# Performance work log

Measured on AMD Instinct MI355X. Metric: run time of the kernel, lower is better.

The kernel has to match this reference:

```python
import jax, jax.numpy as jnp
import numpy as np

N_HEAD = 16


def setup_inputs() -> dict:
    key = jax.random.key(0)
    ks = jax.random.split(key, 3)
    B, T, C = 4, 2048, 1024
    x = jax.random.normal(ks[0], (B, T, C), dtype=jnp.float32)
    w_attn = jax.random.normal(ks[1], (3 * C, C), dtype=jnp.float32) * (1.0 / np.sqrt(C))
    b_attn = jnp.zeros((3 * C,), dtype=jnp.float32)
    w_proj = jax.random.normal(ks[2], (C, C), dtype=jnp.float32) * (1.0 / np.sqrt(C))
    b_proj = jnp.zeros((C,), dtype=jnp.float32)
    return {"x": x, "w_attn": w_attn, "b_attn": b_attn, "w_proj": w_proj, "b_proj": b_proj}


def reference(x, w_attn, b_attn, w_proj, b_proj):
    B, T, C = x.shape
    H = N_HEAD
    D = C // H
    qkv = x @ w_attn.T + b_attn                      # [B, T, 3C]
    q, k, v = jnp.split(qkv, 3, axis=-1)
    # [B, T, C] -> [B, H, T, D]
    q = q.reshape(B, T, H, D).transpose(0, 2, 1, 3)
    k = k.reshape(B, T, H, D).transpose(0, 2, 1, 3)
    v = v.reshape(B, T, H, D).transpose(0, 2, 1, 3)
    scale = 1.0 / np.sqrt(D).astype(np.float32)
    att = jnp.einsum('bhqd,bhkd->bhqk', q, k) * scale  # [B, H, T, T]
    causal = jnp.tril(jnp.ones((T, T), dtype=bool))
    att = jnp.where(causal[None, None], att, -jnp.inf)
    att = jax.nn.softmax(att, axis=-1)
    y = jnp.einsum('bhqk,bhkd->bhqd', att, v)          # [B, H, T, D]
    y = y.transpose(0, 2, 1, 3).reshape(B, T, C)
    return y @ w_proj.T + b_proj
```

## Files before the change

kernel.cpp:

```cpp
#include <hip/hip_runtime.h>
#include <hip/hip_bf16.h>
#include <stdint.h>

typedef __attribute__((ext_vector_type(8))) short bf16x8;
typedef __attribute__((ext_vector_type(4))) float f32x4;

#define MFMA16(a, b, c) __builtin_amdgcn_mfma_f32_16x16x32_bf16((a), (b), (c), 0, 0, 0)

__device__ __forceinline__ unsigned short f2bf(float f) {
  unsigned int u = __builtin_bit_cast(unsigned int, f);
  unsigned int r = (u + 0x7fffu + ((u >> 16) & 1u)) >> 16;
  return (unsigned short)r;
}

__device__ __forceinline__ void gload16(const unsigned short* g, unsigned short* lds_dst) {
  __builtin_amdgcn_global_load_lds(
      (const __attribute__((address_space(1))) unsigned int*)g,
      (__attribute__((address_space(3))) unsigned int*)lds_dst, 16, 0, 0);
}

__global__ void cvt_f32_bf16(const float* __restrict__ in, unsigned short* __restrict__ out, long n) {
  long i = ((long)blockIdx.x * blockDim.x + threadIdx.x) * 4;
  long stride = (long)gridDim.x * blockDim.x * 4;
  for (; i < n; i += stride) {
    float4 v = *(const float4*)(in + i);
    ushort4 o;
    o.x = f2bf(v.x); o.y = f2bf(v.y); o.z = f2bf(v.z); o.w = f2bf(v.w);
    *(ushort4*)(out + i) = o;
  }
}

template <int EPI, int NB>
__global__ __launch_bounds__(512, 2)
void gemm_bt(const unsigned short* __restrict__ A,
             const unsigned short* __restrict__ Bt,
             const float* __restrict__ bias,
             int M, int N, int K,
             unsigned short* __restrict__ q_out,
             unsigned short* __restrict__ k_out,
             unsigned short* __restrict__ vt_out,
             float* __restrict__ f_out) {
  constexpr int BNT = NB * 64;
  alignas(16) __shared__ unsigned short Alds[2][2][128 * 64];
  alignas(16) __shared__ unsigned short Blds[2][BNT * 64];
  const int t = threadIdx.x, w = t >> 6, l = t & 63;
  const int bm = blockIdx.x, bn = blockIdx.y;
  const int wm = w >> 2, wn = w & 3;
  const int lo = l & 15, hi = l >> 4, swk = lo & 7;

  f32x4 acc[8][NB];
  const f32x4 zero = {0.f, 0.f, 0.f, 0.f};
#pragma unroll
  for (int i = 0; i < 8; ++i)
#pragma unroll
    for (int j = 0; j < NB; ++j) acc[i][j] = zero;

  const int sr = t >> 3;
  const int gsrcE = ((t & 7) ^ (sr & 7)) * 8;
  const unsigned short* Asrc = A + (long)(bm * 256 + sr) * K + gsrcE;
  const unsigned short* Bsrc = Bt + (long)(bn * BNT + sr) * K + gsrcE;

#define STAGE_AH(sb, qh, koff) do {                                    \
    unsigned short* d_ = &Alds[sb][qh][w * 512];                       \
    const unsigned short* s_ = Asrc + (long)(qh) * 64 * K + (koff);    \
    gload16(s_, d_); gload16(s_ + 128L * K, d_ + 4096); } while (0)
#define STAGE_B(sb, koff) do {                                         \
    _Pragma("unroll")                                                  \
    for (int c_ = 0; c_ < NB; ++c_)                                    \
      gload16(Bsrc + (long)c_ * 64 * K + (koff),                       \
              &Blds[sb][c_ * 4096 + w * 512]); } while (0)

  STAGE_AH(0, 0, 0);
  STAGE_AH(0, 1, 0);
  STAGE_B(0, 0);
  asm volatile("s_waitcnt vmcnt(0)" ::: "memory");
  __builtin_amdgcn_sched_barrier(0);
  __builtin_amdgcn_s_barrier();

  const int lrA = (wm * 64 + lo) * 64;
  const int lrB = (wn * (NB * 16) + lo) * 64;
  const int gk0 = ((hi) ^ swk) * 8;
  const int gk1 = ((4 + hi) ^ swk) * 8;

  bf16x8 af[4][2], blo[2][2], bhi[2];

  for (int kt = 0; kt < 16; ++kt) {
    const int c = kt & 1, nb = c ^ 1;
    const bool st = (kt < 15);
    const int koff = (kt + 1) * 64;
    const unsigned short* A0 = Alds[c][0];
    const unsigned short* A1 = Alds[c][1];
    const unsigned short* Bs = Blds[c];

#pragma unroll
    for (int ii = 0; ii < 4; ++ii) {
      af[ii][0] = *(const bf16x8*)&A0[lrA + ii * 1024 + gk0];
      af[ii][1] = *(const bf16x8*)&A0[lrA + ii * 1024 + gk1];
    }
#pragma unroll
    for (int jj = 0; jj < NB - 1; ++jj) {
      blo[jj][0] = *(const bf16x8*)&Bs[lrB + jj * 1024 + gk0];
      blo[jj][1] = *(const bf16x8*)&Bs[lrB + jj * 1024 + gk1];
    }
    if (st) STAGE_AH(nb, 0, koff);
    __builtin_amdgcn_s_barrier();
    asm volatile("s_waitcnt lgkmcnt(0)" ::: "memory");
    __builtin_amdgcn_sched_barrier(0);
    __builtin_amdgcn_s_setprio(1);
#pragma unroll
    for (int ii = 0; ii < 4; ++ii)
#pragma unroll
      for (int jj = 0; jj < NB - 1; ++jj) {
        acc[ii][jj] = MFMA16(af[ii][0], blo[jj][0], acc[ii][jj]);
        acc[ii][jj] = MFMA16(af[ii][1], blo[jj][1], acc[ii][jj]);
      }
    __builtin_amdgcn_s_setprio(0);
    __builtin_amdgcn_s_barrier();

    bhi[0] = *(const bf16x8*)&Bs[lrB + (NB - 1) * 1024 + gk0];
    bhi[1] = *(const bf16x8*)&Bs[lrB + (NB - 1) * 1024 + gk1];
    if (st) STAGE_AH(nb, 1, koff);
    __builtin_amdgcn_s_barrier();
    asm volatile("s_waitcnt lgkmcnt(0)" ::: "memory");
    __builtin_amdgcn_sched_barrier(0);
    __builtin_amdgcn_s_setprio(1);
#pragma unroll
    for (int ii = 0; ii < 4; ++ii) {
      acc[ii][NB - 1] = MFMA16(af[ii][0], bhi[0], acc[ii][NB - 1]);
      acc[ii][NB - 1] = MFMA16(af[ii][1], bhi[1], acc[ii][NB - 1]);
    }
    __builtin_amdgcn_s_setprio(0);
    __builtin_amdgcn_s_barrier();

#pragma unroll
    for (int ii = 0; ii < 4; ++ii) {
      af[ii][0] = *(const bf16x8*)&A1[lrA + ii * 1024 + gk0];
      af[ii][1] = *(const bf16x8*)&A1[lrA + ii * 1024 + gk1];
    }
    if (st) STAGE_B(nb, koff);
    __builtin_amdgcn_s_barrier();
    asm volatile("s_waitcnt lgkmcnt(0)" ::: "memory");
    __builtin_amdgcn_sched_barrier(0);
    __builtin_amdgcn_s_setprio(1);
#pragma unroll
    for (int ii = 0; ii < 4; ++ii) {
      acc[4 + ii][NB - 1] = MFMA16(af[ii][0], bhi[0], acc[4 + ii][NB - 1]);
      acc[4 + ii][NB - 1] = MFMA16(af[ii][1], bhi[1], acc[4 + ii][NB - 1]);
    }
    __builtin_amdgcn_s_setprio(0);
    __builtin_amdgcn_s_barrier();

    __builtin_amdgcn_s_setprio(1);
#pragma unroll
    for (int ii = 0; ii < 4; ++ii)
#pragma unroll
      for (int jj = 0; jj < NB - 1; ++jj) {
        acc[4 + ii][jj] = MFMA16(af[ii][0], blo[jj][0], acc[4 + ii][jj]);
        acc[4 + ii][jj] = MFMA16(af[ii][1], blo[jj][1], acc[4 + ii][jj]);
      }
    __builtin_amdgcn_s_setprio(0);
    if (st) {
      asm volatile("s_waitcnt vmcnt(0)" ::: "memory");
      __builtin_amdgcn_sched_barrier(0);
    }
    __builtin_amdgcn_s_barrier();
  }
#undef STAGE_AH
#undef STAGE_B

#pragma unroll
  for (int i = 0; i < 8; ++i) {
#pragma unroll
    for (int j = 0; j < NB; ++j) {
#pragma unroll
      for (int r = 0; r < 4; ++r) {
        int row = bm * 256 + wm * 128 + i * 16 + hi * 4 + r;
        int col = bn * BNT + wn * (NB * 16) + j * 16 + lo;
        float v = acc[i][j][r] + bias[col];
        if (EPI == 0) {
          int b = row >> 11, tt = row & 2047;
          int seg = col >> 10, cc = col & 1023;
          int h = cc >> 6, d = cc & 63;
          long bh = (long)(b * 16 + h);
          if (seg == 0)      q_out[(bh * 2048 + tt) * 64 + d] = f2bf(v * 0.1803368801111f);
          else if (seg == 1) k_out[(bh * 2048 + tt) * 64 + d] = f2bf(v);
          else               vt_out[(bh * 64 + d) * 2048 + tt] = f2bf(v);
        } else {
          f_out[(long)row * N + col] = v;
        }
      }
    }
  }
}

__global__ __launch_bounds__(512, 4)
void attn_kernel(const unsigned short* __restrict__ Q,
                 const unsigned short* __restrict__ K,
                 const unsigned short* __restrict__ Vt,
                 unsigned short* __restrict__ Y) {
  alignas(16) __shared__ unsigned short Kbuf[2][64 * 64];
  alignas(16) __shared__ unsigned short Vbuf[2][64 * 64];
  alignas(16) __shared__ unsigned short pbuf[8][16 * 64];
  const int t = threadIdx.x, w = t >> 6, l = t & 63;
  const int lo = l & 15, hi = l >> 4;
  const int bh = blockIdx.x;
  const int p = blockIdx.y;
  const int b = bh >> 4, h = bh & 15;
  const int sA = p, sB = 15 - p;
  const int nA = 2 * p + 2;
  const int nTot = 34;
  const unsigned short* Qp = Q + (long)bh * 2048 * 64;
  const unsigned short* Kp = K + (long)bh * 2048 * 64;
  const unsigned short* Vp = Vt + (long)bh * 64 * 2048;
  unsigned short* pw = pbuf[w];

  const short one_bf = (short)0x3F80;
  const bf16x8 ones = {one_bf, one_bf, one_bf, one_bf, one_bf, one_bf, one_bf, one_bf};
  const f32x4 zero = {0.f, 0.f, 0.f, 0.f};

  const int qbA = sA * 128 + w * 16;
  const int qbB = sB * 128 + w * 16;

  bf16x8 qf0, qf1;
  f32x4 lsum;
  f32x4 oacc[4];

  qf0 = *(const bf16x8*)&Qp[(qbA + lo) * 64 + hi * 8];
  qf1 = *(const bf16x8*)&Qp[(qbA + lo) * 64 + 32 + hi * 8];
  lsum = zero;
#pragma unroll
  for (int dg = 0; dg < 4; ++dg) oacc[dg] = zero;

  const int srow = t >> 3;
  const int scw = ((t & 7) ^ (srow & 7)) * 8;
  const int sw = lo & 7;

#define STAGE(kvoff, bufidx)                                          \
  do {                                                                \
    unsigned short* KB_ = Kbuf[bufidx] + w * 512;                     \
    unsigned short* VB_ = Vbuf[bufidx] + w * 512;                     \
    gload16(Kp + (long)((kvoff) + srow) * 64 + scw, KB_);             \
    gload16(Vp + (long)srow * 2048 + (kvoff) + scw, VB_);             \
  } while (0)

  STAGE(0, 0);
  __syncthreads();

  for (int g = 0; g < nTot; ++g) {
    const bool inA = (g < nA);
    const int kvb = (inA ? g : g - nA) * 64;
    const int cur = g & 1;
    if (g + 1 < nTot) {
      const int jn = (g + 1 < nA) ? g + 1 : g + 1 - nA;
      STAGE(jn * 64, cur ^ 1);
    }
    const int qbase = inA ? qbA : qbB;
    if (kvb <= qbase + 15) {
      const unsigned short* KB = Kbuf[cur];
      const unsigned short* VB = Vbuf[cur];
      f32x4 s[4];
#pragma unroll
      for (int cg = 0; cg < 4; ++cg) s[cg] = zero;
      __builtin_amdgcn_s_setprio(1);
#pragma unroll
      for (int cg = 0; cg < 4; ++cg) {
        bf16x8 k0 = *(const bf16x8*)&KB[(cg * 16 + lo) * 64 + ((hi) ^ sw) * 8];
        bf16x8 k1 = *(const bf16x8*)&KB[(cg * 16 + lo) * 64 + ((4 + hi) ^ sw) * 8];
        s[cg] = MFMA16(k0, qf0, s[cg]);
        s[cg] = MFMA16(k1, qf1, s[cg]);
      }
      __builtin_amdgcn_s_setprio(0);
      if (kvb + 63 > qbase) {
        const int limit = qbase + lo - kvb;
#pragma unroll
        for (int cg = 0; cg < 4; ++cg)
#pragma unroll
          for (int r = 0; r < 4; ++r)
            if (cg * 16 + hi * 4 + r > limit) s[cg][r] = -__builtin_inff();
      }
#pragma unroll
      for (int cg = 0; cg < 4; ++cg) {
        float p0 = exp2f(s[cg][0]);
        float p1 = exp2f(s[cg][1]);
        float p2 = exp2f(s[cg][2]);
        float p3 = exp2f(s[cg][3]);
        unsigned int u0, u1;
        asm("v_cvt_pk_bf16_f32 %0, %1, %2" : "=v"(u0) : "v"(p0), "v"(p1));
        asm("v_cvt_pk_bf16_f32 %0, %1, %2" : "=v"(u1) : "v"(p2), "v"(p3));
        const int gg = (cg * 2 + (hi >> 1)) ^ sw;
        uint2 val; val.x = u0; val.y = u1;
        *(uint2*)&pw[lo * 64 + gg * 8 + (hi & 1) * 4] = val;
      }
      asm volatile("s_waitcnt lgkmcnt(0)" ::: "memory");
      bf16x8 pa0 = *(const bf16x8*)&pw[lo * 64 + ((hi) ^ sw) * 8];
      bf16x8 pa1 = *(const bf16x8*)&pw[lo * 64 + ((4 + hi) ^ sw) * 8];
      __builtin_amdgcn_s_setprio(1);
      lsum = MFMA16(pa0, ones, lsum);
      lsum = MFMA16(pa1, ones, lsum);
#pragma unroll
      for (int dg = 0; dg < 4; ++dg) {
        bf16x8 vv0 = *(const bf16x8*)&VB[(dg * 16 + lo) * 64 + ((hi) ^ sw) * 8];
        bf16x8 vv1 = *(const bf16x8*)&VB[(dg * 16 + lo) * 64 + ((4 + hi) ^ sw) * 8];
        oacc[dg] = MFMA16(pa0, vv0, oacc[dg]);
        oacc[dg] = MFMA16(pa1, vv1, oacc[dg]);
      }
      __builtin_amdgcn_s_setprio(0);
    }
    if (g == nA - 1) {
#pragma unroll
      for (int r = 0; r < 4; ++r) {
        float inv = 1.0f / lsum[r];
        int rowg = qbA + hi * 4 + r;
        long base = ((long)b * 2048 + rowg) * 1024 + h * 64;
#pragma unroll
        for (int dg = 0; dg < 4; ++dg)
          Y[base + dg * 16 + lo] = f2bf(oacc[dg][r] * inv);
      }
      qf0 = *(const bf16x8*)&Qp[(qbB + lo) * 64 + hi * 8];
      qf1 = *(const bf16x8*)&Qp[(qbB + lo) * 64 + 32 + hi * 8];
      lsum = zero;
#pragma unroll
      for (int dg = 0; dg < 4; ++dg) oacc[dg] = zero;
    }
    __syncthreads();
  }

#pragma unroll
  for (int r = 0; r < 4; ++r) {
    float inv = 1.0f / lsum[r];
    int rowg = qbB + hi * 4 + r;
    long base = ((long)b * 2048 + rowg) * 1024 + h * 64;
#pragma unroll
    for (int dg = 0; dg < 4; ++dg)
      Y[base + dg * 16 + lo] = f2bf(oacc[dg][r] * inv);
  }
#undef STAGE
}

extern "C" void kernel_launch(void* const* d_in, const int* in_sizes, int n_in,
                              void* d_out, int out_size, void* d_ws, size_t ws_size,
                              hipStream_t stream) {
  const float* x      = (const float*)d_in[0];
  const float* w_attn = (const float*)d_in[1];
  const float* b_attn = (const float*)d_in[2];
  const float* w_proj = (const float*)d_in[3];
  const float* b_proj = (const float*)d_in[4];
  float* out = (float*)d_out;

  const long NX = 8192L * 1024;
  const long NWA = 3072L * 1024;
  const long NWP = 1024L * 1024;
  const long NQ = 64L * 2048 * 64;

  char* ws = (char*)d_ws;
  unsigned short* xb  = (unsigned short*)ws; ws += NX * 2;
  unsigned short* wab = (unsigned short*)ws; ws += NWA * 2;
  unsigned short* wpb = (unsigned short*)ws; ws += NWP * 2;
  unsigned short* qb  = (unsigned short*)ws; ws += NQ * 2;
  unsigned short* kb  = (unsigned short*)ws; ws += NQ * 2;
  unsigned short* vtb = (unsigned short*)ws; ws += NQ * 2;
  unsigned short* yb  = (unsigned short*)ws; ws += NX * 2;

  cvt_f32_bf16<<<2048, 256, 0, stream>>>(x, xb, NX);
  cvt_f32_bf16<<<768, 256, 0, stream>>>(w_attn, wab, NWA);
  cvt_f32_bf16<<<256, 256, 0, stream>>>(w_proj, wpb, NWP);

  dim3 g1(32, 16);
  gemm_bt<0, 3><<<g1, 512, 0, stream>>>(xb, wab, b_attn, 8192, 3072, 1024,
                                        qb, kb, vtb, nullptr);
  dim3 ga(64, 8);
  attn_kernel<<<ga, 512, 0, stream>>>(qb, kb, vtb, yb);
  dim3 g2(32, 8);
  gemm_bt<1, 2><<<g2, 512, 0, stream>>>(yb, wpb, b_proj, 8192, 1024, 1024,
                                        nullptr, nullptr, nullptr, out);
}
```

Before: 181.7 us.

## Shrink GEMM M-tile to 128 and simplify the double-buffered pipeline

The GEMM block tile drops from 256 to 128 rows, the launch grid doubles, and the kernel now asks for 4 blocks per CU instead of 2. The four-phase, barrier-heavy interleaved schedule becomes one prefetch-then-compute loop per K step. The aim is more occupancy, fewer barriers, lower register and LDS use, and more blocks to spread across CUs. In exchange, each block reuses the B tile over half as many rows, so global and L2 traffic for B doubles. The hand-tuned overlap of LDS reads with MFMA is also lost.

```diff
diff --git a/kernel.cpp b/kernel.cpp
--- a/kernel.cpp
+++ b/kernel.cpp
@@ -31,7 +31,7 @@
 }
 
 template <int EPI, int NB>
-__global__ __launch_bounds__(512, 2)
+__global__ __launch_bounds__(512, 4)
 void gemm_bt(const unsigned short* __restrict__ A,
              const unsigned short* __restrict__ Bt,
              const float* __restrict__ bias,
@@ -41,40 +41,38 @@
              unsigned short* __restrict__ vt_out,
              float* __restrict__ f_out) {
   constexpr int BNT = NB * 64;
-  alignas(16) __shared__ unsigned short Alds[2][2][128 * 64];
+  alignas(16) __shared__ unsigned short Alds[2][128 * 64];
   alignas(16) __shared__ unsigned short Blds[2][BNT * 64];
   const int t = threadIdx.x, w = t >> 6, l = t & 63;
   const int bm = blockIdx.x, bn = blockIdx.y;
   const int wm = w >> 2, wn = w & 3;
   const int lo = l & 15, hi = l >> 4, swk = lo & 7;
 
-  f32x4 acc[8][NB];
+  f32x4 acc[4][NB];
   const f32x4 zero = {0.f, 0.f, 0.f, 0.f};
 #pragma unroll
-  for (int i = 0; i < 8; ++i)
+  for (int i = 0; i < 4; ++i)
 #pragma unroll
     for (int j = 0; j < NB; ++j) acc[i][j] = zero;
 
   const int sr = t >> 3;
   const int gsrcE = ((t & 7) ^ (sr & 7)) * 8;
-  const unsigned short* Asrc = A + (long)(bm * 256 + sr) * K + gsrcE;
+  const unsigned short* Asrc = A + (long)(bm * 128 + sr) * K + gsrcE;
   const unsigned short* Bsrc = Bt + (long)(bn * BNT + sr) * K + gsrcE;
 
-#define STAGE_AH(sb, qh, koff) do {                                    \
-    unsigned short* d_ = &Alds[sb][qh][w * 512];                       \
-    const unsigned short* s_ = Asrc + (long)(qh) * 64 * K + (koff);    \
-    gload16(s_, d_); gload16(s_ + 128L * K, d_ + 4096); } while (0)
-#define STAGE_B(sb, koff) do {                                         \
-    _Pragma("unroll")                                                  \
-    for (int c_ = 0; c_ < NB; ++c_)                                    \
-      gload16(Bsrc + (long)c_ * 64 * K + (koff),                       \
+#define STAGE_A(sb, koff) do {                                \
+    unsigned short* d_ = &Alds[sb][w * 512];                  \
+    gload16(Asrc + (koff), d_);                               \
+    gload16(Asrc + 64L * K + (koff), d_ + 4096); } while (0)
+#define STAGE_B(sb, koff) do {                                \
+    _Pragma("unroll")                                         \
+    for (int c_ = 0; c_ < NB; ++c_)                           \
+      gload16(Bsrc + (long)c_ * 64 * K + (koff),              \
               &Blds[sb][c_ * 4096 + w * 512]); } while (0)
 
-  STAGE_AH(0, 0, 0);
-  STAGE_AH(0, 1, 0);
+  STAGE_A(0, 0);
   STAGE_B(0, 0);
   asm volatile("s_waitcnt vmcnt(0)" ::: "memory");
-  __builtin_amdgcn_sched_barrier(0);
   __builtin_amdgcn_s_barrier();
 
   const int lrA = (wm * 64 + lo) * 64;
@@ -82,99 +80,53 @@
   const int gk0 = ((hi) ^ swk) * 8;
   const int gk1 = ((4 + hi) ^ swk) * 8;
 
-  bf16x8 af[4][2], blo[2][2], bhi[2];
-
   for (int kt = 0; kt < 16; ++kt) {
-    const int c = kt & 1, nb = c ^ 1;
+    const int cur = kt & 1, nb = cur ^ 1;
     const bool st = (kt < 15);
     const int koff = (kt + 1) * 64;
-    const unsigned short* A0 = Alds[c][0];
-    const unsigned short* A1 = Alds[c][1];
-    const unsigned short* Bs = Blds[c];
-
-#pragma unroll
-    for (int ii = 0; ii < 4; ++ii) {
-      af[ii][0] = *(const bf16x8*)&A0[lrA + ii * 1024 + gk0];
-      af[ii][1] = *(const bf16x8*)&A0[lrA + ii * 1024 + gk1];
-    }
-#pragma unroll
-    for (int jj = 0; jj < NB - 1; ++jj) {
-      blo[jj][0] = *(const bf16x8*)&Bs[lrB + jj * 1024 + gk0];
-      blo[jj][1] = *(const bf16x8*)&Bs[lrB + jj * 1024 + gk1];
-    }
-    if (st) STAGE_AH(nb, 0, koff);
+    const unsigned short* As = Alds[cur];
+    const unsigned short* Bs = Blds[cur];
+
+    if (st) { STAGE_A(nb, koff); STAGE_B(nb, koff); }
+
+    bf16x8 bfr[NB][2];
+#pragma unroll
+    for (int jj = 0; jj < NB; ++jj) {
+      bfr[jj][0] = *(const bf16x8*)&Bs[lrB + jj * 1024 + gk0];
+      bfr[jj][1] = *(const bf16x8*)&Bs[lrB + jj * 1024 + gk1];
+    }
+#pragma unroll
+    for (int ih = 0; ih < 2; ++ih) {
+      bf16x8 af[2][2];
+#pragma unroll
+      for (int ii = 0; ii < 2; ++ii) {
+        af[ii][0] = *(const bf16x8*)&As[lrA + (ih * 2 + ii) * 1024 + gk0];
+        af[ii][1] = *(const bf16x8*)&As[lrA + (ih * 2 + ii) * 1024 + gk1];
+      }
+      __builtin_amdgcn_s_setprio(1);
+#pragma unroll
+      for (int ii = 0; ii < 2; ++ii)
+#pragma unroll
+        for (int jj = 0; jj < NB; ++jj) {
+          acc[ih * 2 + ii][jj] = MFMA16(af[ii][0], bfr[jj][0], acc[ih * 2 + ii][jj]);
+          acc[ih * 2 + ii][jj] = MFMA16(af[ii][1], bfr[jj][1], acc[ih * 2 + ii][jj]);
+        }
+      __builtin_amdgcn_s_setprio(0);
+    }
+
+    if (st) { asm volatile("s_waitcnt vmcnt(0)" ::: "memory"); }
     __builtin_amdgcn_s_barrier();
-    asm volatile("s_waitcnt lgkmcnt(0)" ::: "memory");
-    __builtin_amdgcn_sched_barrier(0);
-    __builtin_amdgcn_s_setprio(1);
-#pragma unroll
-    for (int ii = 0; ii < 4; ++ii)
-#pragma unroll
-      for (int jj = 0; jj < NB - 1; ++jj) {
-        acc[ii][jj] = MFMA16(af[ii][0], blo[jj][0], acc[ii][jj]);
-        acc[ii][jj] = MFMA16(af[ii][1], blo[jj][1], acc[ii][jj]);
-      }
-    __builtin_amdgcn_s_setprio(0);
-    __builtin_amdgcn_s_barrier();
-
-    bhi[0] = *(const bf16x8*)&Bs[lrB + (NB - 1) * 1024 + gk0];
-    bhi[1] = *(const bf16x8*)&Bs[lrB + (NB - 1) * 1024 + gk1];
-    if (st) STAGE_AH(nb, 1, koff);
-    __builtin_amdgcn_s_barrier();
-    asm volatile("s_waitcnt lgkmcnt(0)" ::: "memory");
-    __builtin_amdgcn_sched_barrier(0);
-    __builtin_amdgcn_s_setprio(1);
-#pragma unroll
-    for (int ii = 0; ii < 4; ++ii) {
-      acc[ii][NB - 1] = MFMA16(af[ii][0], bhi[0], acc[ii][NB - 1]);
-      acc[ii][NB - 1] = MFMA16(af[ii][1], bhi[1], acc[ii][NB - 1]);
-    }
-    __builtin_amdgcn_s_setprio(0);
-    __builtin_amdgcn_s_barrier();
-
-#pragma unroll
-    for (int ii = 0; ii < 4; ++ii) {
-      af[ii][0] = *(const bf16x8*)&A1[lrA + ii * 1024 + gk0];
-      af[ii][1] = *(const bf16x8*)&A1[lrA + ii * 1024 + gk1];
-    }
-    if (st) STAGE_B(nb, koff);
-    __builtin_amdgcn_s_barrier();
-    asm volatile("s_waitcnt lgkmcnt(0)" ::: "memory");
-    __builtin_amdgcn_sched_barrier(0);
-    __builtin_amdgcn_s_setprio(1);
-#pragma unroll
-    for (int ii = 0; ii < 4; ++ii) {
-      acc[4 + ii][NB - 1] = MFMA16(af[ii][0], bhi[0], acc[4 + ii][NB - 1]);
-      acc[4 + ii][NB - 1] = MFMA16(af[ii][1], bhi[1], acc[4 + ii][NB - 1]);
-    }
-    __builtin_amdgcn_s_setprio(0);
-    __builtin_amdgcn_s_barrier();
-
-    __builtin_amdgcn_s_setprio(1);
-#pragma unroll
-    for (int ii = 0; ii < 4; ++ii)
-#pragma unroll
-      for (int jj = 0; jj < NB - 1; ++jj) {
-        acc[4 + ii][jj] = MFMA16(af[ii][0], blo[jj][0], acc[4 + ii][jj]);
-        acc[4 + ii][jj] = MFMA16(af[ii][1], blo[jj][1], acc[4 + ii][jj]);
-      }
-    __builtin_amdgcn_s_setprio(0);
-    if (st) {
-      asm volatile("s_waitcnt vmcnt(0)" ::: "memory");
-      __builtin_amdgcn_sched_barrier(0);
-    }
-    __builtin_amdgcn_s_barrier();
-  }
-#undef STAGE_AH
+  }
+#undef STAGE_A
 #undef STAGE_B
 
 #pragma unroll
-  for (int i = 0; i < 8; ++i) {
+  for (int i = 0; i < 4; ++i) {
 #pragma unroll
     for (int j = 0; j < NB; ++j) {
 #pragma unroll
       for (int r = 0; r < 4; ++r) {
-        int row = bm * 256 + wm * 128 + i * 16 + hi * 4 + r;
+        int row = bm * 128 + wm * 64 + i * 16 + hi * 4 + r;
         int col = bn * BNT + wn * (NB * 16) + j * 16 + lo;
         float v = acc[i][j][r] + bias[col];
         if (EPI == 0) {
@@ -365,12 +317,12 @@
   cvt_f32_bf16<<<768, 256, 0, stream>>>(w_attn, wab, NWA);
   cvt_f32_bf16<<<256, 256, 0, stream>>>(w_proj, wpb, NWP);
 
-  dim3 g1(32, 16);
+  dim3 g1(64, 16);
   gemm_bt<0, 3><<<g1, 512, 0, stream>>>(xb, wab, b_attn, 8192, 3072, 1024,
                                         qb, kb, vtb, nullptr);
   dim3 ga(64, 8);
   attn_kernel<<<ga, 512, 0, stream>>>(qb, kb, vtb, yb);
-  dim3 g2(32, 8);
+  dim3 g2(64, 8);
   gemm_bt<1, 2><<<g2, 512, 0, stream>>>(yb, wpb, b_proj, 8192, 1024, 1024,
                                         nullptr, nullptr, nullptr, out);
 }
```

After: 181.3 us. About the same (-0.2%).
